# Performance work log

Hardware: AMD Instinct MI355X
Metric: run time of the kernel (lower is better)

## Reference

```python
import jax, jax.numpy as jnp
import numpy as np

NP, NR, NK = 64, 8, 500          # problems, rollouts, candidate nodes
H, HEADS, VD = 256, 8, 8         # hidden_dim, heads, vars_dim
HD = H // HEADS                  # head_dim
CLIP = 10.0                      # tanh logit clipping
NEG_INF = -jnp.inf


def setup_inputs() -> dict:
    key = jax.random.key(0)
    ks = jax.random.split(key, 17)
    f = lambda k, s: jax.random.normal(k, s, dtype=jnp.float32)
    B = NP * NR
    s = 1.0 / np.sqrt(H)
    return {
        "X": f(ks[0], (NP, NK, H)),
        "K": f(ks[1], (HEADS, NP, NK, HD)),
        "V": f(ks[2], (HEADS, NP, NK, HD)),
        "query": f(ks[3], (B, H)),
        "state1": f(ks[4], (B, H)),
        "state2": f(ks[5], (B, H)),
        "varfeat": f(ks[6], (NP, VD, NK)),
        "mask": jax.random.uniform(ks[7], (NP, NR, NK)) < 0.1,
        "nn_Q": f(ks[8], (HEADS, H, HD)) * (1.0 / np.sqrt(HD)),
        "nn_O": f(ks[9], (H, H)) * s,
        "nn_A": f(ks[10], (VD, H)) * s,
        "nn_B": f(ks[11], (H,)) * s,
        "nn_W": f(ks[12], (H,)) * s,
        "W_ih": f(ks[13], (4 * H, H)) * s,
        "W_hh": f(ks[14], (4 * H, H)) * s,
        "b_ih": f(ks[15], (4 * H,)) * s,
        "b_hh": f(ks[16], (4 * H,)) * s,
    }


def _decode(X, K, V, query, state1, state2, varfeat, mask,
            nn_Q, nn_O, nn_A, nn_B, nn_W, W_ih, W_hh, b_ih, b_hh):
    B = query.shape[0]
    # --- LSTMCell (PyTorch gate order: i, f, g, o) ---
    gates = query @ W_ih.T + b_ih + state1 @ W_hh.T + b_hh
    i, fg, g, o = jnp.split(gates, 4, axis=1)
    c = jax.nn.sigmoid(fg) * state2 + jax.nn.sigmoid(i) * jnp.tanh(g)
    h = jax.nn.sigmoid(o) * jnp.tanh(c)
    # --- MultiHeadAttention (glimpse) ---
    q = h.reshape(NP, NR, H)
    Q = jnp.einsum('pqh,ahd->apqd', q, nn_Q)                    # [heads,NP,NR,HD]
    S = jnp.einsum('apqd,apkd->apqk', Q, K) * (1.0 / np.sqrt(HD))
    S = jnp.where(mask[None], NEG_INF, S)
    S = jax.nn.softmax(S, axis=-1)
    x = jnp.einsum('apqk,apkd->apqd', S, V)
    x = x.transpose(1, 2, 0, 3).reshape(NP, NR, H)              # [NP,NR,H]
    qm = x @ nn_O                                               # glimpse query
    # --- additive attention with variable features ---
    vf = jnp.einsum('pvk,vh->pkh', varfeat, nn_A) + nn_B        # [NP,NK,H]
    t = jnp.tanh(X[:, None] + vf[:, None] + qm[:, :, None])     # [NP,NR,NK,H]
    logit = jnp.einsum('pqkh,h->pqk', t, nn_W)
    logit = jnp.where(mask, NEG_INF, logit).reshape(B, NK)
    # --- choose (mode=1: greedy argmax) ---
    infeasible = logit == NEG_INF
    l = jnp.where(infeasible, NEG_INF, jnp.tanh(logit) * CLIP)
    chosen = jnp.argmax(l, axis=1)
    logp = jax.nn.log_softmax(l, axis=1)
    chosen_p = jnp.take_along_axis(logp, chosen[:, None], axis=1).squeeze(1)
    return h, c, chosen_p


def reference(X, K, V, query, state1, state2, varfeat, mask,
              nn_Q, nn_O, nn_A, nn_B, nn_W, W_ih, W_hh, b_ih, b_hh):
    return _decode(X, K, V, query, state1, state2, varfeat, mask,
                   nn_Q, nn_O, nn_A, nn_B, nn_W, W_ih, W_hh, b_ih, b_hh)
```

## Files before the change

kernel.cpp:

```cpp
#include <hip/hip_runtime.h>

#define NPP   64
#define NRR   8
#define NKK   500
#define HDIM  256
#define NHEAD 8
#define VDIM  8
#define HD    32
#define BTOT  512

__device__ __forceinline__ float fast_tanh(float x) {
  const float e = __expf(2.f * x);
  return 1.f - 2.f * __builtin_amdgcn_rcpf(e + 1.f);
}
__device__ __forceinline__ float fast_sig(float x) {
  return __builtin_amdgcn_rcpf(1.f + __expf(-x));
}

__global__ __launch_bounds__(256) void k_lstm3(
    const float* __restrict__ query, const float* __restrict__ state1,
    const float* __restrict__ state2,
    const float* __restrict__ W_ih, const float* __restrict__ W_hh,
    const float* __restrict__ b_ih, const float* __restrict__ b_hh,
    const unsigned char* __restrict__ maskb, int* __restrict__ flagp,
    float* __restrict__ out_h, float* __restrict__ out_c)
{
  __shared__ float Wt[32][33];
  __shared__ float At[32][33];
  __shared__ float gt[32][33];

  const int t  = threadIdx.x;
  const int hb = blockIdx.x;
  const int bb = blockIdx.y;

  if (flagp != nullptr && hb == 0 && bb == 0) {
    __shared__ int f;
    if (t == 0) f = 0;
    __syncthreads();
    int any = 0;
    for (int j = t; j < 2048; j += 256) any |= maskb[2 * j + 1];
    if (any) atomicOr(&f, 1);
    __syncthreads();
    if (t == 0) *flagp = f;
  }

  const int trow = t >> 4;
  const int tcol = t & 15;

  float acc00 = 0.f, acc01 = 0.f, acc10 = 0.f, acc11 = 0.f;

  const int wrow = t >> 3, wk4 = t & 7;
  const int wpart = wrow >> 3, whh = wrow & 7;
  const int wgrow = wpart * HDIM + hb * 8 + whh;
  const int agrow = bb * 32 + wrow;

  for (int k0 = 0; k0 < 512; k0 += 32) {
    __syncthreads();
    {
      const float* wsrc = (k0 < 256) ? (W_ih + (size_t)wgrow * HDIM + k0)
                                     : (W_hh + (size_t)wgrow * HDIM + (k0 - 256));
      const float4 wv = *reinterpret_cast<const float4*>(wsrc + wk4 * 4);
      Wt[wk4 * 4 + 0][wrow] = wv.x; Wt[wk4 * 4 + 1][wrow] = wv.y;
      Wt[wk4 * 4 + 2][wrow] = wv.z; Wt[wk4 * 4 + 3][wrow] = wv.w;

      const float* asrc = (k0 < 256) ? (query  + (size_t)agrow * HDIM + k0)
                                     : (state1 + (size_t)agrow * HDIM + (k0 - 256));
      const float4 av = *reinterpret_cast<const float4*>(asrc + wk4 * 4);
      At[wk4 * 4 + 0][wrow] = av.x; At[wk4 * 4 + 1][wrow] = av.y;
      At[wk4 * 4 + 2][wrow] = av.z; At[wk4 * 4 + 3][wrow] = av.w;
    }
    __syncthreads();

#pragma unroll 8
    for (int kk = 0; kk < 32; ++kk) {
      const float w0 = Wt[kk][trow], w1 = Wt[kk][trow + 16];
      const float a0 = At[kk][tcol], a1 = At[kk][tcol + 16];
      acc00 += w0 * a0; acc01 += w0 * a1;
      acc10 += w1 * a0; acc11 += w1 * a1;
    }
  }

  gt[trow][tcol] = acc00;      gt[trow][tcol + 16] = acc01;
  gt[trow + 16][tcol] = acc10; gt[trow + 16][tcol + 16] = acc11;
  __syncthreads();

  {
    const int h = t & 7, b = t >> 3;
    const int gh = hb * 8 + h;
    const int gb = bb * 32 + b;
    const float bi = b_ih[0 * HDIM + gh] + b_hh[0 * HDIM + gh];
    const float bf = b_ih[1 * HDIM + gh] + b_hh[1 * HDIM + gh];
    const float bg = b_ih[2 * HDIM + gh] + b_hh[2 * HDIM + gh];
    const float bo = b_ih[3 * HDIM + gh] + b_hh[3 * HDIM + gh];
    const float iv = fast_sig (gt[ 0 + h][b] + bi);
    const float fv = fast_sig (gt[ 8 + h][b] + bf);
    const float gv = fast_tanh(gt[16 + h][b] + bg);
    const float ov = fast_sig (gt[24 + h][b] + bo);
    const size_t off = (size_t)gb * HDIM + gh;
    const float c = fv * state2[off] + iv * gv;
    out_c[off] = c;
    out_h[off] = ov * fast_tanh(c);
  }
}

__global__ __launch_bounds__(1024) void k_attn6(
    const float* __restrict__ Kt, const float* __restrict__ Vt,
    const float* __restrict__ nn_Q, const float* __restrict__ nn_O,
    const void* __restrict__ maskp, const int* __restrict__ flagp,
    const float* __restrict__ out_h, float* __restrict__ qmw, int use_slabs)
{
  const int p = blockIdx.x >> 3;
  const int a = blockIdx.x & 7;
  const int t = threadIdx.x;
  const int wave = t >> 6, lane = t & 63;

  __shared__ float hs[NRR][HDIM];
  __shared__ float buf[HDIM * 33];
  __shared__ float Qs[NRR][HD];
  __shared__ float Sb[NRR][NKK];
  __shared__ float xs[NRR][HD];

  const unsigned char* mb = (const unsigned char*)maskp;
  const int* mi = (const int*)maskp;

  float4 hv = make_float4(0.f, 0.f, 0.f, 0.f);
  if (t < 512)
    hv = reinterpret_cast<const float4*>(out_h + (size_t)p * NRR * HDIM)[t];
  const float4* nq4 = reinterpret_cast<const float4*>(nn_Q + (size_t)a * HDIM * HD);
  const float4 q0 = nq4[t];
  const float4 q1 = nq4[t + 1024];

  const int flag = *flagp;

  const int k2 = t >> 1, dh = t & 1;
  const int kc = (k2 < NKK) ? k2 : (NKK - 1);
  const float4 kreg = *reinterpret_cast<const float4*>(
      Kt + (((size_t)a * NPP + p) * NKK + kc) * HD + dh * 16);

  const int dpv = t & 31, kspv = t >> 5;
  const float* vb = Vt + ((size_t)a * NPP + p) * NKK * HD + dpv;
  float vreg[16];
#pragma unroll
  for (int j = 0; j < 15; ++j) vreg[j] = vb[(size_t)(kspv + 32 * j) * HD];
  vreg[15] = (kspv < NKK - 480) ? vb[(size_t)(kspv + 480) * HD] : 0.f;

  float maskval[NRR];
#pragma unroll
  for (int r = 0; r < NRR; ++r) maskval[r] = 0.f;
  if (dh == 0 && k2 < NKK) {
    if (flag) {
#pragma unroll
      for (int r = 0; r < NRR; ++r)
        maskval[r] = mb[(size_t)(p * NRR + r) * NKK + k2] ? -INFINITY : 0.f;
    } else {
#pragma unroll
      for (int r = 0; r < NRR; ++r)
        maskval[r] = mi[(size_t)(p * NRR + r) * NKK + k2] ? -INFINITY : 0.f;
    }
  }

  if (t < 512) reinterpret_cast<float4*>(&hs[0][0])[t] = hv;
  {
    const int h0 = t >> 3, d40 = t & 7;
    buf[h0 * 33 + d40 * 4 + 0] = q0.x; buf[h0 * 33 + d40 * 4 + 1] = q0.y;
    buf[h0 * 33 + d40 * 4 + 2] = q0.z; buf[h0 * 33 + d40 * 4 + 3] = q0.w;
    const int h1 = (t + 1024) >> 3, d41 = t & 7;
    buf[h1 * 33 + d41 * 4 + 0] = q1.x; buf[h1 * 33 + d41 * 4 + 1] = q1.y;
    buf[h1 * 33 + d41 * 4 + 2] = q1.z; buf[h1 * 33 + d41 * 4 + 3] = q1.w;
  }
  __syncthreads();

  {
    const int r = t >> 7, d = (t >> 2) & 31, c = t & 3;
    float acc = 0.f;
#pragma unroll 8
    for (int h = c * 64; h < c * 64 + 64; ++h)
      acc += hs[r][h] * buf[h * 33 + d];
    float* qp = &Sb[0][0];
    qp[((r * HD) + d) * 4 + c] = acc;
  }
  __syncthreads();
  if (t < 256) {
    const int r = t >> 5, d = t & 31;
    const float* qp = &Sb[0][0];
    Qs[r][d] = (qp[(r * HD + d) * 4 + 0] + qp[(r * HD + d) * 4 + 1]
              + qp[(r * HD + d) * 4 + 2] + qp[(r * HD + d) * 4 + 3])
             * 0.17677669529663687f;
  }
  __syncthreads();

  {
    float sc[NRR];
#pragma unroll
    for (int r = 0; r < NRR; ++r) sc[r] = 0.f;
#pragma unroll
    for (int c4 = 0; c4 < 4; ++c4) {
      const float u[4] = {c4 == 0 ? kreg.x : (c4 == 1 ? kreg.x : kreg.x)};
      (void)u;
    }
    {
      const float4 u = kreg;
#pragma unroll
      for (int r = 0; r < NRR; ++r) {
        sc[r] += Qs[r][dh * 16 + 0] * u.x + Qs[r][dh * 16 + 1] * u.y
               + Qs[r][dh * 16 + 2] * u.z + Qs[r][dh * 16 + 3] * u.w;
      }
    }
    const float4* kr4 = reinterpret_cast<const float4*>(
        Kt + (((size_t)a * NPP + p) * NKK + kc) * HD + dh * 16);
    const float4 u1 = kr4[1], u2 = kr4[2], u3 = kr4[3];
#pragma unroll
    for (int r = 0; r < NRR; ++r) {
      sc[r] += Qs[r][dh * 16 +  4] * u1.x + Qs[r][dh * 16 +  5] * u1.y
             + Qs[r][dh * 16 +  6] * u1.z + Qs[r][dh * 16 +  7] * u1.w
             + Qs[r][dh * 16 +  8] * u2.x + Qs[r][dh * 16 +  9] * u2.y
             + Qs[r][dh * 16 + 10] * u2.z + Qs[r][dh * 16 + 11] * u2.w
             + Qs[r][dh * 16 + 12] * u3.x + Qs[r][dh * 16 + 13] * u3.y
             + Qs[r][dh * 16 + 14] * u3.z + Qs[r][dh * 16 + 15] * u3.w;
    }
#pragma unroll
    for (int r = 0; r < NRR; ++r) sc[r] += __shfl_xor(sc[r], 1, 64);
    if (dh == 0 && k2 < NKK) {
#pragma unroll
      for (int r = 0; r < NRR; ++r)
        Sb[r][k2] = sc[r] + maskval[r];
    }
  }
  __syncthreads();

  if (wave < NRR) {
    const int r = wave;
    float m = -INFINITY;
    for (int k = lane; k < NKK; k += 64) m = fmaxf(m, Sb[r][k]);
#pragma unroll
    for (int off = 32; off > 0; off >>= 1) m = fmaxf(m, __shfl_xor(m, off, 64));
    float ssum = 0.f;
    for (int k = lane; k < NKK; k += 64) {
      const float e = __expf(Sb[r][k] - m);
      Sb[r][k] = e;
      ssum += e;
    }
#pragma unroll
    for (int off = 32; off > 0; off >>= 1) ssum += __shfl_xor(ssum, off, 64);
    const float inv = 1.f / ssum;
    for (int k = lane; k < NKK; k += 64) Sb[r][k] *= inv;
  }
  __syncthreads();

  {
    float acc[NRR];
#pragma unroll
    for (int r = 0; r < NRR; ++r) acc[r] = 0.f;
#pragma unroll
    for (int j = 0; j < 15; ++j) {
      const int k = kspv + 32 * j;
      const float v = vreg[j];
#pragma unroll
      for (int r = 0; r < NRR; ++r) acc[r] += Sb[r][k] * v;
    }
    if (kspv < NKK - 480) {
      const int k = kspv + 480;
      const float v = vreg[15];
#pragma unroll
      for (int r = 0; r < NRR; ++r) acc[r] += Sb[r][k] * v;
    }
#pragma unroll
    for (int r = 0; r < NRR; ++r) buf[(kspv * NRR + r) * HD + dpv] = acc[r];
  }
  __syncthreads();
  if (t < 256) {
    const int r = t >> 5, d = t & 31;
    float s = 0.f;
#pragma unroll
    for (int ks = 0; ks < 32; ++ks) s += buf[(ks * NRR + r) * HD + d];
    xs[r][d] = s;
  }
  __syncthreads();

  {
    const int j = t & 255, rr = t >> 8;
    const int r0 = rr * 2;
    float a0 = 0.f, a1 = 0.f;
#pragma unroll 8
    for (int d = 0; d < HD; ++d) {
      const float w = nn_O[((size_t)(a * HD + d)) * HDIM + j];
      a0 += xs[r0][d] * w;
      a1 += xs[r0 + 1][d] * w;
    }
    if (use_slabs) {
      float* slab = qmw + (size_t)a * BTOT * HDIM;
      slab[(size_t)(p * NRR + r0) * HDIM + j] = a0;
      slab[(size_t)(p * NRR + r0 + 1) * HDIM + j] = a1;
    } else {
      atomicAdd(&qmw[(size_t)(p * NRR + r0) * HDIM + j], a0);
      atomicAdd(&qmw[(size_t)(p * NRR + r0 + 1) * HDIM + j], a1);
    }
  }
}

__global__ __launch_bounds__(256) void k_logits4(
    const float* __restrict__ X, const float* __restrict__ varfeat,
    const float* __restrict__ nn_A, const float* __restrict__ nn_B,
    const float* __restrict__ nn_W, const float* __restrict__ qmw,
    int use_slabs, const int* __restrict__ flagp,
    const void* __restrict__ maskp, float* __restrict__ ls)
{
  const int p  = blockIdx.x >> 5;
  const int kt = blockIdx.x & 31;
  const int t = threadIdx.x;
  const int wave = t >> 6, lane = t & 63;
  const int h0 = lane * 4;

  __shared__ float As[VDIM][260];
  __shared__ float Ws[HDIM];
  __shared__ float qb[NRR][260];

  const unsigned char* mb = (const unsigned char*)maskp;
  const int* mi = (const int*)maskp;

  const int flag = *flagp;

  for (int idx = t; idx < VDIM * HDIM; idx += 256)
    As[idx >> 8][idx & 255] = nn_A[idx];
  Ws[t] = nn_W[t];
  for (int idx = t; idx < NRR * HDIM; idx += 256) {
    const int r = idx >> 8, h = idx & 255;
    float q;
    if (use_slabs) {
      q = 0.f;
#pragma unroll
      for (int a = 0; a < NHEAD; ++a)
        q += qmw[(size_t)a * BTOT * HDIM + (size_t)(p * NRR + r) * HDIM + h];
    } else {
      q = qmw[(size_t)(p * NRR + r) * HDIM + h];
    }
    qb[r][h] = q + nn_B[h];
  }
  __syncthreads();
  const bool mbyte = (flag != 0);

  const float4 w4 = *reinterpret_cast<const float4*>(&Ws[h0]);

  for (int kk = 0; kk < 4; ++kk) {
    const int k = kt * 16 + wave * 4 + kk;
    if (k >= NKK) break;

    const float4 x4 = *reinterpret_cast<const float4*>(
        X + ((size_t)p * NKK + k) * HDIM + h0);
    float base0 = x4.x, base1 = x4.y, base2 = x4.z, base3 = x4.w;
#pragma unroll
    for (int v = 0; v < VDIM; ++v) {
      const float vv = varfeat[((size_t)p * VDIM + v) * NKK + k];
      const float4 a4 = *reinterpret_cast<const float4*>(&As[v][h0]);
      base0 += vv * a4.x; base1 += vv * a4.y;
      base2 += vv * a4.z; base3 += vv * a4.w;
    }

    float acc[NRR];
#pragma unroll
    for (int r = 0; r < NRR; ++r) {
      const float4 q4 = *reinterpret_cast<const float4*>(&qb[r][h0]);
      acc[r] = fast_tanh(base0 + q4.x) * w4.x + fast_tanh(base1 + q4.y) * w4.y
             + fast_tanh(base2 + q4.z) * w4.z + fast_tanh(base3 + q4.w) * w4.w;
    }

    float v4[4];
    {
      float sw[8];
#pragma unroll
      for (int j = 0; j < 8; ++j) sw[j] = __shfl_xor(acc[j], 32, 64);
      const bool hi = (lane & 32) != 0;
#pragma unroll
      for (int j = 0; j < 4; ++j)
        v4[j] = hi ? (acc[j + 4] + sw[j + 4]) : (acc[j] + sw[j]);
    }
    float v2[2];
    {
      float sw[4];
#pragma unroll
      for (int j = 0; j < 4; ++j) sw[j] = __shfl_xor(v4[j], 16, 64);
      const bool hi = (lane & 16) != 0;
      v2[0] = hi ? (v4[2] + sw[2]) : (v4[0] + sw[0]);
      v2[1] = hi ? (v4[3] + sw[3]) : (v4[1] + sw[1]);
    }
    float w;
    {
      const float s0 = __shfl_xor(v2[0], 8, 64);
      const float s1 = __shfl_xor(v2[1], 8, 64);
      w = ((lane & 8) != 0) ? (v2[1] + s1) : (v2[0] + s0);
    }
    w += __shfl_xor(w, 4, 64);
    w += __shfl_xor(w, 2, 64);
    w += __shfl_xor(w, 1, 64);

    if ((lane & 7) == 0) {
      const int r = lane >> 3;
      const size_t mrow = (size_t)(p * NRR + r) * NKK + k;
      const bool mk = mbyte ? (mb[mrow] != 0) : (mi[mrow] != 0);
      ls[mrow] = mk ? -INFINITY : fast_tanh(w) * 10.0f;
    }
  }
}

__global__ __launch_bounds__(64) void k_choose(
    const float* __restrict__ ls, float* __restrict__ out_p)
{
  const int b = blockIdx.x;
  const int lane = threadIdx.x;
  float m = -INFINITY;
  float lv[8];
  int n = 0;
  for (int k = lane; k < NKK; k += 64, ++n) {
    lv[n] = ls[(size_t)b * NKK + k];
    m = fmaxf(m, lv[n]);
  }
#pragma unroll
  for (int off = 32; off > 0; off >>= 1) m = fmaxf(m, __shfl_xor(m, off, 64));
  float s = 0.f;
  for (int i = 0; i < n; ++i) s += __expf(lv[i] - m);
#pragma unroll
  for (int off = 32; off > 0; off >>= 1) s += __shfl_xor(s, off, 64);
  if (lane == 0) out_p[b] = -logf(s);
}

__global__ __launch_bounds__(256) void k_fused(
    const float* __restrict__ X, const float* __restrict__ Kt,
    const float* __restrict__ Vt, const float* __restrict__ varfeat,
    const void* __restrict__ maskp,
    const float* __restrict__ nn_Q, const float* __restrict__ nn_O,
    const float* __restrict__ nn_A, const float* __restrict__ nn_B,
    const float* __restrict__ nn_W,
    const float* __restrict__ out_h, float* __restrict__ out_p)
{
  const int p = blockIdx.x >> 3;
  const int r = blockIdx.x & 7;
  const int t = threadIdx.x;
  const int wave = t >> 6, lane = t & 63;

  __shared__ float hs[HDIM];
  __shared__ float Qs[NHEAD][HD];
  __shared__ float Sb[NHEAD][NKK];
  __shared__ float xs[HDIM];
  __shared__ float qs[HDIM];
  __shared__ float As2[HDIM][VDIM];
  __shared__ float Ws[HDIM];
  __shared__ float lsb[NKK];
  __shared__ int   mask_any;

  const unsigned char* mb = (const unsigned char*)maskp;
  if (t == 0) mask_any = 0;
  __syncthreads();
  {
    int any = 0;
    for (int j = t; j < 2048; j += 256) any |= mb[2 * j + 1];
    if (any) atomicOr(&mask_any, 1);
  }
  for (int idx = t; idx < VDIM * HDIM; idx += 256)
    As2[idx & 255][idx >> 8] = nn_A[idx];
  Ws[t] = nn_W[t];
  hs[t] = out_h[(size_t)(p * NRR + r) * HDIM + t];
  __syncthreads();
  const bool mbyte = (mask_any != 0);
  const int* mi = (const int*)maskp;
  const size_t mrow = (size_t)(p * NRR + r) * NKK;
  {
    const int a = t >> 5, d = t & 31;
    const float* nq = nn_Q + (size_t)a * HDIM * HD + d;
    float acc = 0.f;
    for (int h = 0; h < HDIM; ++h) acc += hs[h] * nq[(size_t)h * HD];
    Qs[a][d] = acc * 0.17677669529663687f;
  }
  __syncthreads();
  for (int k = t; k < NKK; k += 256) {
    const bool mk = mbyte ? (mb[mrow + k] != 0) : (mi[mrow + k] != 0);
#pragma unroll
    for (int a = 0; a < NHEAD; ++a) {
      const float4* kr4 = reinterpret_cast<const float4*>(
          Kt + (((size_t)a * NPP + p) * NKK + k) * HD);
      float s = 0.f;
#pragma unroll
      for (int d4 = 0; d4 < HD / 4; ++d4) {
        const float4 u = kr4[d4];
        s += Qs[a][4 * d4] * u.x + Qs[a][4 * d4 + 1] * u.y
           + Qs[a][4 * d4 + 2] * u.z + Qs[a][4 * d4 + 3] * u.w;
      }
      Sb[a][k] = mk ? -INFINITY : s;
    }
  }
  __syncthreads();
  for (int aa = 0; aa < 2; ++aa) {
    const int a = wave * 2 + aa;
    float m = -INFINITY;
    for (int k = lane; k < NKK; k += 64) m = fmaxf(m, Sb[a][k]);
#pragma unroll
    for (int off = 32; off > 0; off >>= 1) m = fmaxf(m, __shfl_xor(m, off, 64));
    float ssum = 0.f;
    for (int k = lane; k < NKK; k += 64) {
      const float e = expf(Sb[a][k] - m);
      Sb[a][k] = e; ssum += e;
    }
#pragma unroll
    for (int off = 32; off > 0; off >>= 1) ssum += __shfl_xor(ssum, off, 64);
    const float inv = 1.f / ssum;
    for (int k = lane; k < NKK; k += 64) Sb[a][k] *= inv;
  }
  __syncthreads();
  {
    const int a = t >> 5, d = t & 31;
    const float* vb = Vt + ((size_t)a * NPP + p) * NKK * HD + d;
    float acc = 0.f;
    for (int k = 0; k < NKK; ++k) acc += Sb[a][k] * vb[(size_t)k * HD];
    xs[a * HD + d] = acc;
  }
  __syncthreads();
  {
    float acc = 0.f;
    for (int i = 0; i < HDIM; ++i) acc += xs[i] * nn_O[(size_t)i * HDIM + t];
    qs[t] = acc + nn_B[t];
  }
  __syncthreads();
  for (int k = t; k < NKK; k += 256) {
    float vfv[VDIM];
#pragma unroll
    for (int v = 0; v < VDIM; ++v)
      vfv[v] = varfeat[((size_t)p * VDIM + v) * NKK + k];
    const float4* xp4 = reinterpret_cast<const float4*>(
        X + ((size_t)p * NKK + k) * HDIM);
    float acc = 0.f;
    for (int h4 = 0; h4 < HDIM / 4; ++h4) {
      const float4 ux = xp4[h4];
      const float xv[4] = {ux.x, ux.y, ux.z, ux.w};
#pragma unroll
      for (int j = 0; j < 4; ++j) {
        const int h = 4 * h4 + j;
        float base = xv[j] + qs[h];
        const float4 a0 = *reinterpret_cast<const float4*>(&As2[h][0]);
        const float4 a1 = *reinterpret_cast<const float4*>(&As2[h][4]);
        base += vfv[0] * a0.x + vfv[1] * a0.y + vfv[2] * a0.z + vfv[3] * a0.w
              + vfv[4] * a1.x + vfv[5] * a1.y + vfv[6] * a1.z + vfv[7] * a1.w;
        acc += tanhf(base) * Ws[h];
      }
    }
    lsb[k] = acc;
  }
  __syncthreads();
  for (int k = t; k < NKK; k += 256) {
    const bool mk = mbyte ? (mb[mrow + k] != 0) : (mi[mrow + k] != 0);
    lsb[k] = mk ? -INFINITY : tanhf(lsb[k]) * 10.0f;
  }
  __syncthreads();
  if (wave == 0) {
    float m = -INFINITY;
    for (int k = lane; k < NKK; k += 64) m = fmaxf(m, lsb[k]);
#pragma unroll
    for (int off = 32; off > 0; off >>= 1) m = fmaxf(m, __shfl_xor(m, off, 64));
    float s = 0.f;
    for (int k = lane; k < NKK; k += 64) s += expf(lsb[k] - m);
#pragma unroll
    for (int off = 32; off > 0; off >>= 1) s += __shfl_xor(s, off, 64);
    if (lane == 0) out_p[p * NRR + r] = -logf(s);
  }
}

extern "C" void kernel_launch(void* const* d_in, const int* in_sizes, int n_in,
                              void* d_out, int out_size, void* d_ws, size_t ws_size,
                              hipStream_t stream)
{
  const float* X       = (const float*)d_in[0];
  const float* Kt      = (const float*)d_in[1];
  const float* Vt      = (const float*)d_in[2];
  const float* query   = (const float*)d_in[3];
  const float* state1  = (const float*)d_in[4];
  const float* state2  = (const float*)d_in[5];
  const float* varfeat = (const float*)d_in[6];
  const void*  maskp   = d_in[7];
  const float* nn_Q    = (const float*)d_in[8];
  const float* nn_O    = (const float*)d_in[9];
  const float* nn_A    = (const float*)d_in[10];
  const float* nn_B    = (const float*)d_in[11];
  const float* nn_W    = (const float*)d_in[12];
  const float* W_ih    = (const float*)d_in[13];
  const float* W_hh    = (const float*)d_in[14];
  const float* b_ih    = (const float*)d_in[15];
  const float* b_hh    = (const float*)d_in[16];

  float* out   = (float*)d_out;
  float* out_h = out;
  float* out_c = out + (size_t)BTOT * HDIM;
  float* out_p = out + (size_t)2 * BTOT * HDIM;

  const size_t flag_bytes = 256;
  const size_t qm1_bytes  = (size_t)BTOT * HDIM * 4;
  const size_t qm8_bytes  = (size_t)NHEAD * BTOT * HDIM * 4;
  const size_t ls_bytes   = (size_t)BTOT * NKK * 4;

  const bool slabs  = ws_size >= flag_bytes + qm8_bytes + ls_bytes;
  const bool atomic = !slabs && ws_size >= flag_bytes + qm1_bytes + ls_bytes;
  int* flagp = (slabs || atomic) ? (int*)d_ws : nullptr;

  hipLaunchKernelGGL(k_lstm3, dim3(32, 16), dim3(256), 0, stream,
                     query, state1, state2, W_ih, W_hh, b_ih, b_hh,
                     (const unsigned char*)maskp, flagp, out_h, out_c);

  if (slabs || atomic) {
    float* qmw = (float*)((char*)d_ws + flag_bytes);
    float* lsw = (float*)((char*)d_ws + flag_bytes +
                          (slabs ? qm8_bytes : qm1_bytes));
    const int use_slabs = slabs ? 1 : 0;
    if (!slabs) hipMemsetAsync(qmw, 0, qm1_bytes, stream);
    hipLaunchKernelGGL(k_attn6, dim3(NPP * NHEAD), dim3(1024), 0, stream,
                       Kt, Vt, nn_Q, nn_O, maskp, flagp, out_h, qmw, use_slabs);
    hipLaunchKernelGGL(k_logits4, dim3(NPP * 32), dim3(256), 0, stream,
                       X, varfeat, nn_A, nn_B, nn_W, qmw, use_slabs, flagp,
                       maskp, lsw);
    hipLaunchKernelGGL(k_choose, dim3(BTOT), dim3(64), 0, stream,
                       lsw, out_p);
  } else {
    hipLaunchKernelGGL(k_fused, dim3(NPP * NRR), dim3(256), 0, stream,
                       X, Kt, Vt, varfeat, maskp,
                       nn_Q, nn_O, nn_A, nn_B, nn_W,
                       out_h, out_p);
  }
}
```

Measured before the change: 222.1 us.

## Split attention projections into standalone GEMMs and register-tile LSTM GEMM

Moves the per-head Q projection and the output projection out of the attention kernel into a reusable 32x32 register-tiled GEMM kernel. The attention kernel shrinks to 512 threads, keeps full K/V rows in registers and writes the per-head context to workspace. The LSTM GEMM now uses 64-thread blocks with 4x4 register tiles. The logits kernel reads weights straight into registers instead of staging them in shared memory. The aim is to cut redundant per-block projection work, the slab reduction and shared-memory traffic, at the cost of two extra launches and extra workspace round trips.

```diff
diff --git a/kernel.cpp b/kernel.cpp
--- a/kernel.cpp
+++ b/kernel.cpp
@@ -17,7 +17,7 @@
   return __builtin_amdgcn_rcpf(1.f + __expf(-x));
 }
 
-__global__ __launch_bounds__(256) void k_lstm3(
+__global__ __launch_bounds__(64) void k_lstm4(
     const float* __restrict__ query, const float* __restrict__ state1,
     const float* __restrict__ state2,
     const float* __restrict__ W_ih, const float* __restrict__ W_hh,
@@ -25,9 +25,9 @@
     const unsigned char* __restrict__ maskb, int* __restrict__ flagp,
     float* __restrict__ out_h, float* __restrict__ out_c)
 {
-  __shared__ float Wt[32][33];
-  __shared__ float At[32][33];
-  __shared__ float gt[32][33];
+  __shared__ float Wt[32][40];
+  __shared__ float At[32][40];
+  __shared__ float gt[32][40];
 
   const int t  = threadIdx.x;
   const int hb = blockIdx.x;
@@ -38,54 +38,67 @@
     if (t == 0) f = 0;
     __syncthreads();
     int any = 0;
-    for (int j = t; j < 2048; j += 256) any |= maskb[2 * j + 1];
+    for (int j = t; j < 2048; j += 64) any |= maskb[2 * j + 1];
     if (any) atomicOr(&f, 1);
     __syncthreads();
     if (t == 0) *flagp = f;
   }
 
-  const int trow = t >> 4;
-  const int tcol = t & 15;
-
-  float acc00 = 0.f, acc01 = 0.f, acc10 = 0.f, acc11 = 0.f;
-
-  const int wrow = t >> 3, wk4 = t & 7;
-  const int wpart = wrow >> 3, whh = wrow & 7;
-  const int wgrow = wpart * HDIM + hb * 8 + whh;
-  const int agrow = bb * 32 + wrow;
+  const int tr = t >> 3, tc = t & 7;
+  const int srow = t >> 1, sseg = (t & 1) * 16;
+  const int wgrow = (srow >> 3) * HDIM + hb * 8 + (srow & 7);
+  const int agrow = bb * 32 + srow;
+
+  float acc[4][4];
+#pragma unroll
+  for (int i = 0; i < 4; ++i)
+#pragma unroll
+    for (int j = 0; j < 4; ++j) acc[i][j] = 0.f;
 
   for (int k0 = 0; k0 < 512; k0 += 32) {
     __syncthreads();
     {
       const float* wsrc = (k0 < 256) ? (W_ih + (size_t)wgrow * HDIM + k0)
                                      : (W_hh + (size_t)wgrow * HDIM + (k0 - 256));
-      const float4 wv = *reinterpret_cast<const float4*>(wsrc + wk4 * 4);
-      Wt[wk4 * 4 + 0][wrow] = wv.x; Wt[wk4 * 4 + 1][wrow] = wv.y;
-      Wt[wk4 * 4 + 2][wrow] = wv.z; Wt[wk4 * 4 + 3][wrow] = wv.w;
-
       const float* asrc = (k0 < 256) ? (query  + (size_t)agrow * HDIM + k0)
                                      : (state1 + (size_t)agrow * HDIM + (k0 - 256));
-      const float4 av = *reinterpret_cast<const float4*>(asrc + wk4 * 4);
-      At[wk4 * 4 + 0][wrow] = av.x; At[wk4 * 4 + 1][wrow] = av.y;
-      At[wk4 * 4 + 2][wrow] = av.z; At[wk4 * 4 + 3][wrow] = av.w;
+#pragma unroll
+      for (int j = 0; j < 4; ++j) {
+        const float4 wv = *reinterpret_cast<const float4*>(wsrc + sseg + 4 * j);
+        const float4 av = *reinterpret_cast<const float4*>(asrc + sseg + 4 * j);
+        const int kk = sseg + 4 * j;
+        Wt[kk + 0][srow] = wv.x; Wt[kk + 1][srow] = wv.y;
+        Wt[kk + 2][srow] = wv.z; Wt[kk + 3][srow] = wv.w;
+        At[kk + 0][srow] = av.x; At[kk + 1][srow] = av.y;
+        At[kk + 2][srow] = av.z; At[kk + 3][srow] = av.w;
+      }
     }
     __syncthreads();
-
 #pragma unroll 8
     for (int kk = 0; kk < 32; ++kk) {
-      const float w0 = Wt[kk][trow], w1 = Wt[kk][trow + 16];
-      const float a0 = At[kk][tcol], a1 = At[kk][tcol + 16];
-      acc00 += w0 * a0; acc01 += w0 * a1;
-      acc10 += w1 * a0; acc11 += w1 * a1;
-    }
-  }
-
-  gt[trow][tcol] = acc00;      gt[trow][tcol + 16] = acc01;
-  gt[trow + 16][tcol] = acc10; gt[trow + 16][tcol + 16] = acc11;
-  __syncthreads();
-
-  {
-    const int h = t & 7, b = t >> 3;
+      const float4 wv = *reinterpret_cast<const float4*>(&Wt[kk][tr * 4]);
+      const float4 av = *reinterpret_cast<const float4*>(&At[kk][tc * 4]);
+      const float w[4] = {wv.x, wv.y, wv.z, wv.w};
+      const float a[4] = {av.x, av.y, av.z, av.w};
+#pragma unroll
+      for (int i = 0; i < 4; ++i)
+#pragma unroll
+        for (int j = 0; j < 4; ++j) acc[i][j] += w[i] * a[j];
+    }
+  }
+
+#pragma unroll
+  for (int i = 0; i < 4; ++i) {
+    float4 v;
+    v.x = acc[i][0]; v.y = acc[i][1]; v.z = acc[i][2]; v.w = acc[i][3];
+    *reinterpret_cast<float4*>(&gt[tr * 4 + i][tc * 4]) = v;
+  }
+  __syncthreads();
+
+#pragma unroll
+  for (int it = 0; it < 4; ++it) {
+    const int cell = t + 64 * it;
+    const int b = cell & 31, h = cell >> 5;
     const int gh = hb * 8 + h;
     const int gb = bb * 32 + b;
     const float bi = b_ih[0 * HDIM + gh] + b_hh[0 * HDIM + gh];
@@ -103,147 +116,139 @@
   }
 }
 
-__global__ __launch_bounds__(1024) void k_attn6(
+__global__ __launch_bounds__(64) void k_gemm256(
+    const float* __restrict__ A, const float* __restrict__ B,
+    float* __restrict__ C, int hstride, int ldb, float scale)
+{
+  __shared__ float At[32][40];
+  __shared__ float Bt[32][40];
+  const int t  = threadIdx.x;
+  const int ct = blockIdx.x;
+  const int rt = blockIdx.y;
+  const int tr = t >> 3, tc = t & 7;
+  const int srow = t >> 1, sseg = (t & 1) * 16;
+
+  const float* Asrc = A + ((size_t)(rt * 32 + srow)) * HDIM + sseg;
+  const float* Bsrc = B + (size_t)hstride * ct + (size_t)srow * ldb + sseg;
+
+  float acc[4][4];
+#pragma unroll
+  for (int i = 0; i < 4; ++i)
+#pragma unroll
+    for (int j = 0; j < 4; ++j) acc[i][j] = 0.f;
+
+  for (int k0 = 0; k0 < 256; k0 += 32) {
+    __syncthreads();
+#pragma unroll
+    for (int j = 0; j < 4; ++j) {
+      const float4 av = *reinterpret_cast<const float4*>(Asrc + k0 + 4 * j);
+      const int kk = sseg + 4 * j;
+      At[kk + 0][srow] = av.x; At[kk + 1][srow] = av.y;
+      At[kk + 2][srow] = av.z; At[kk + 3][srow] = av.w;
+      const float4 bv = *reinterpret_cast<const float4*>(
+          Bsrc + (size_t)k0 * ldb + 4 * j);
+      *reinterpret_cast<float4*>(&Bt[srow][sseg + 4 * j]) = bv;
+    }
+    __syncthreads();
+#pragma unroll 8
+    for (int kk = 0; kk < 32; ++kk) {
+      const float4 av = *reinterpret_cast<const float4*>(&At[kk][tr * 4]);
+      const float4 bv = *reinterpret_cast<const float4*>(&Bt[kk][tc * 4]);
+      const float a[4] = {av.x, av.y, av.z, av.w};
+      const float b[4] = {bv.x, bv.y, bv.z, bv.w};
+#pragma unroll
+      for (int i = 0; i < 4; ++i)
+#pragma unroll
+        for (int j = 0; j < 4; ++j) acc[i][j] += a[i] * b[j];
+    }
+  }
+
+  const int orow = rt * 32 + tr * 4;
+  const int ocol = ct * 32 + tc * 4;
+#pragma unroll
+  for (int i = 0; i < 4; ++i) {
+    float4 v;
+    v.x = acc[i][0] * scale; v.y = acc[i][1] * scale;
+    v.z = acc[i][2] * scale; v.w = acc[i][3] * scale;
+    *reinterpret_cast<float4*>(C + (size_t)(orow + i) * HDIM + ocol) = v;
+  }
+}
+
+__global__ __launch_bounds__(512, 4) void k_attn7(
     const float* __restrict__ Kt, const float* __restrict__ Vt,
-    const float* __restrict__ nn_Q, const float* __restrict__ nn_O,
-    const void* __restrict__ maskp, const int* __restrict__ flagp,
-    const float* __restrict__ out_h, float* __restrict__ qmw, int use_slabs)
+    const float* __restrict__ Qg, const void* __restrict__ maskp,
+    const int* __restrict__ flagp, float* __restrict__ xg)
 {
   const int p = blockIdx.x >> 3;
   const int a = blockIdx.x & 7;
   const int t = threadIdx.x;
   const int wave = t >> 6, lane = t & 63;
 
-  __shared__ float hs[NRR][HDIM];
-  __shared__ float buf[HDIM * 33];
-  __shared__ float Qs[NRR][HD];
-  __shared__ float Sb[NRR][NKK];
-  __shared__ float xs[NRR][HD];
-
-  const unsigned char* mb = (const unsigned char*)maskp;
-  const int* mi = (const int*)maskp;
-
-  float4 hv = make_float4(0.f, 0.f, 0.f, 0.f);
-  if (t < 512)
-    hv = reinterpret_cast<const float4*>(out_h + (size_t)p * NRR * HDIM)[t];
-  const float4* nq4 = reinterpret_cast<const float4*>(nn_Q + (size_t)a * HDIM * HD);
-  const float4 q0 = nq4[t];
-  const float4 q1 = nq4[t + 1024];
+  __shared__ float Sb[NRR][512];
+  __shared__ float pb[16][NRR][HD];
+
+  const int kc = (t < NKK) ? t : (NKK - 1);
+  const float4* kp4 = reinterpret_cast<const float4*>(
+      Kt + (((size_t)a * NPP + p) * NKK + kc) * HD);
+  float4 kreg[8];
+#pragma unroll
+  for (int j = 0; j < 8; ++j) kreg[j] = kp4[j];
+
+  const int dpv = t & 31, kb = t >> 5;
+  const float* vb = Vt + (((size_t)a * NPP + p) * NKK + (size_t)kb * 32) * HD + dpv;
+  float vreg[32];
+#pragma unroll
+  for (int j = 0; j < 32; ++j)
+    vreg[j] = (kb * 32 + j < NKK) ? vb[(size_t)j * HD] : 0.f;
 
   const int flag = *flagp;
-
-  const int k2 = t >> 1, dh = t & 1;
-  const int kc = (k2 < NKK) ? k2 : (NKK - 1);
-  const float4 kreg = *reinterpret_cast<const float4*>(
-      Kt + (((size_t)a * NPP + p) * NKK + kc) * HD + dh * 16);
-
-  const int dpv = t & 31, kspv = t >> 5;
-  const float* vb = Vt + ((size_t)a * NPP + p) * NKK * HD + dpv;
-  float vreg[16];
-#pragma unroll
-  for (int j = 0; j < 15; ++j) vreg[j] = vb[(size_t)(kspv + 32 * j) * HD];
-  vreg[15] = (kspv < NKK - 480) ? vb[(size_t)(kspv + 480) * HD] : 0.f;
-
-  float maskval[NRR];
-#pragma unroll
-  for (int r = 0; r < NRR; ++r) maskval[r] = 0.f;
-  if (dh == 0 && k2 < NKK) {
-    if (flag) {
-#pragma unroll
-      for (int r = 0; r < NRR; ++r)
-        maskval[r] = mb[(size_t)(p * NRR + r) * NKK + k2] ? -INFINITY : 0.f;
-    } else {
-#pragma unroll
-      for (int r = 0; r < NRR; ++r)
-        maskval[r] = mi[(size_t)(p * NRR + r) * NKK + k2] ? -INFINITY : 0.f;
-    }
-  }
-
-  if (t < 512) reinterpret_cast<float4*>(&hs[0][0])[t] = hv;
-  {
-    const int h0 = t >> 3, d40 = t & 7;
-    buf[h0 * 33 + d40 * 4 + 0] = q0.x; buf[h0 * 33 + d40 * 4 + 1] = q0.y;
-    buf[h0 * 33 + d40 * 4 + 2] = q0.z; buf[h0 * 33 + d40 * 4 + 3] = q0.w;
-    const int h1 = (t + 1024) >> 3, d41 = t & 7;
-    buf[h1 * 33 + d41 * 4 + 0] = q1.x; buf[h1 * 33 + d41 * 4 + 1] = q1.y;
-    buf[h1 * 33 + d41 * 4 + 2] = q1.z; buf[h1 * 33 + d41 * 4 + 3] = q1.w;
-  }
-  __syncthreads();
-
-  {
-    const int r = t >> 7, d = (t >> 2) & 31, c = t & 3;
-    float acc = 0.f;
-#pragma unroll 8
-    for (int h = c * 64; h < c * 64 + 64; ++h)
-      acc += hs[r][h] * buf[h * 33 + d];
-    float* qp = &Sb[0][0];
-    qp[((r * HD) + d) * 4 + c] = acc;
-  }
-  __syncthreads();
-  if (t < 256) {
-    const int r = t >> 5, d = t & 31;
-    const float* qp = &Sb[0][0];
-    Qs[r][d] = (qp[(r * HD + d) * 4 + 0] + qp[(r * HD + d) * 4 + 1]
-              + qp[(r * HD + d) * 4 + 2] + qp[(r * HD + d) * 4 + 3])
-             * 0.17677669529663687f;
-  }
-  __syncthreads();
-
-  {
-    float sc[NRR];
-#pragma unroll
-    for (int r = 0; r < NRR; ++r) sc[r] = 0.f;
-#pragma unroll
-    for (int c4 = 0; c4 < 4; ++c4) {
-      const float u[4] = {c4 == 0 ? kreg.x : (c4 == 1 ? kreg.x : kreg.x)};
-      (void)u;
-    }
-    {
-      const float4 u = kreg;
-#pragma unroll
-      for (int r = 0; r < NRR; ++r) {
-        sc[r] += Qs[r][dh * 16 + 0] * u.x + Qs[r][dh * 16 + 1] * u.y
-               + Qs[r][dh * 16 + 2] * u.z + Qs[r][dh * 16 + 3] * u.w;
-      }
-    }
-    const float4* kr4 = reinterpret_cast<const float4*>(
-        Kt + (((size_t)a * NPP + p) * NKK + kc) * HD + dh * 16);
-    const float4 u1 = kr4[1], u2 = kr4[2], u3 = kr4[3];
+  float maskv[NRR];
+  {
+    const unsigned char* mb = (const unsigned char*)maskp;
+    const int* mi = (const int*)maskp;
 #pragma unroll
     for (int r = 0; r < NRR; ++r) {
-      sc[r] += Qs[r][dh * 16 +  4] * u1.x + Qs[r][dh * 16 +  5] * u1.y
-             + Qs[r][dh * 16 +  6] * u1.z + Qs[r][dh * 16 +  7] * u1.w
-             + Qs[r][dh * 16 +  8] * u2.x + Qs[r][dh * 16 +  9] * u2.y
-             + Qs[r][dh * 16 + 10] * u2.z + Qs[r][dh * 16 + 11] * u2.w
-             + Qs[r][dh * 16 + 12] * u3.x + Qs[r][dh * 16 + 13] * u3.y
-             + Qs[r][dh * 16 + 14] * u3.z + Qs[r][dh * 16 + 15] * u3.w;
-    }
-#pragma unroll
-    for (int r = 0; r < NRR; ++r) sc[r] += __shfl_xor(sc[r], 1, 64);
-    if (dh == 0 && k2 < NKK) {
-#pragma unroll
-      for (int r = 0; r < NRR; ++r)
-        Sb[r][k2] = sc[r] + maskval[r];
-    }
-  }
-  __syncthreads();
-
-  if (wave < NRR) {
+      const size_t mo = (size_t)(p * NRR + r) * NKK + kc;
+      const bool mk = flag ? (mb[mo] != 0) : (mi[mo] != 0);
+      maskv[r] = mk ? -INFINITY : 0.f;
+    }
+  }
+
+#pragma unroll
+  for (int r = 0; r < NRR; ++r) {
+    const float4* q4 = reinterpret_cast<const float4*>(
+        Qg + ((size_t)(p * NRR + r)) * HDIM + a * HD);
+    float s = 0.f;
+#pragma unroll
+    for (int j = 0; j < 8; ++j) {
+      const float4 q = q4[j], k4 = kreg[j];
+      s += q.x * k4.x + q.y * k4.y + q.z * k4.z + q.w * k4.w;
+    }
+    Sb[r][t] = (t < NKK) ? (s + maskv[r]) : -INFINITY;
+  }
+  __syncthreads();
+
+  {
     const int r = wave;
-    float m = -INFINITY;
-    for (int k = lane; k < NKK; k += 64) m = fmaxf(m, Sb[r][k]);
+    float lv[8], m = -INFINITY;
+#pragma unroll
+    for (int i = 0; i < 8; ++i) {
+      lv[i] = Sb[r][lane + 64 * i];
+      m = fmaxf(m, lv[i]);
+    }
 #pragma unroll
     for (int off = 32; off > 0; off >>= 1) m = fmaxf(m, __shfl_xor(m, off, 64));
     float ssum = 0.f;
-    for (int k = lane; k < NKK; k += 64) {
-      const float e = __expf(Sb[r][k] - m);
-      Sb[r][k] = e;
-      ssum += e;
+#pragma unroll
+    for (int i = 0; i < 8; ++i) {
+      lv[i] = __expf(lv[i] - m);
+      ssum += lv[i];
     }
 #pragma unroll
     for (int off = 32; off > 0; off >>= 1) ssum += __shfl_xor(ssum, off, 64);
     const float inv = 1.f / ssum;
-    for (int k = lane; k < NKK; k += 64) Sb[r][k] *= inv;
+#pragma unroll
+    for (int i = 0; i < 8; ++i) Sb[r][lane + 64 * i] = lv[i] * inv;
   }
   __syncthreads();
 
@@ -252,58 +257,36 @@
 #pragma unroll
     for (int r = 0; r < NRR; ++r) acc[r] = 0.f;
 #pragma unroll
-    for (int j = 0; j < 15; ++j) {
-      const int k = kspv + 32 * j;
-      const float v = vreg[j];
-#pragma unroll
-      for (int r = 0; r < NRR; ++r) acc[r] += Sb[r][k] * v;
-    }
-    if (kspv < NKK - 480) {
-      const int k = kspv + 480;
-      const float v = vreg[15];
-#pragma unroll
-      for (int r = 0; r < NRR; ++r) acc[r] += Sb[r][k] * v;
-    }
-#pragma unroll
-    for (int r = 0; r < NRR; ++r) buf[(kspv * NRR + r) * HD + dpv] = acc[r];
-  }
-  __syncthreads();
+    for (int j4 = 0; j4 < 8; ++j4) {
+      const float v0 = vreg[j4 * 4 + 0], v1 = vreg[j4 * 4 + 1];
+      const float v2 = vreg[j4 * 4 + 2], v3 = vreg[j4 * 4 + 3];
+#pragma unroll
+      for (int r = 0; r < NRR; ++r) {
+        const float4 s4 = *reinterpret_cast<const float4*>(
+            &Sb[r][kb * 32 + j4 * 4]);
+        acc[r] += s4.x * v0 + s4.y * v1 + s4.z * v2 + s4.w * v3;
+      }
+    }
+#pragma unroll
+    for (int r = 0; r < NRR; ++r) pb[kb][r][dpv] = acc[r];
+  }
+  __syncthreads();
+
   if (t < 256) {
     const int r = t >> 5, d = t & 31;
     float s = 0.f;
 #pragma unroll
-    for (int ks = 0; ks < 32; ++ks) s += buf[(ks * NRR + r) * HD + d];
-    xs[r][d] = s;
-  }
-  __syncthreads();
-
-  {
-    const int j = t & 255, rr = t >> 8;
-    const int r0 = rr * 2;
-    float a0 = 0.f, a1 = 0.f;
-#pragma unroll 8
-    for (int d = 0; d < HD; ++d) {
-      const float w = nn_O[((size_t)(a * HD + d)) * HDIM + j];
-      a0 += xs[r0][d] * w;
-      a1 += xs[r0 + 1][d] * w;
-    }
-    if (use_slabs) {
-      float* slab = qmw + (size_t)a * BTOT * HDIM;
-      slab[(size_t)(p * NRR + r0) * HDIM + j] = a0;
-      slab[(size_t)(p * NRR + r0 + 1) * HDIM + j] = a1;
-    } else {
-      atomicAdd(&qmw[(size_t)(p * NRR + r0) * HDIM + j], a0);
-      atomicAdd(&qmw[(size_t)(p * NRR + r0 + 1) * HDIM + j], a1);
-    }
-  }
-}
-
-__global__ __launch_bounds__(256) void k_logits4(
+    for (int q = 0; q < 16; ++q) s += pb[q][r][d];
+    xg[((size_t)(p * NRR + r)) * HDIM + a * HD + d] = s;
+  }
+}
+
+__global__ __launch_bounds__(256) void k_logits5(
     const float* __restrict__ X, const float* __restrict__ varfeat,
     const float* __restrict__ nn_A, const float* __restrict__ nn_B,
-    const float* __restrict__ nn_W, const float* __restrict__ qmw,
-    int use_slabs, const int* __restrict__ flagp,
-    const void* __restrict__ maskp, float* __restrict__ ls)
+    const float* __restrict__ nn_W, const float* __restrict__ qm,
+    const int* __restrict__ flagp, const void* __restrict__ maskp,
+    float* __restrict__ ls)
 {
   const int p  = blockIdx.x >> 5;
   const int kt = blockIdx.x & 31;
@@ -311,35 +294,25 @@
   const int wave = t >> 6, lane = t & 63;
   const int h0 = lane * 4;
 
-  __shared__ float As[VDIM][260];
-  __shared__ float Ws[HDIM];
-  __shared__ float qb[NRR][260];
-
   const unsigned char* mb = (const unsigned char*)maskp;
   const int* mi = (const int*)maskp;
-
   const int flag = *flagp;
-
-  for (int idx = t; idx < VDIM * HDIM; idx += 256)
-    As[idx >> 8][idx & 255] = nn_A[idx];
-  Ws[t] = nn_W[t];
-  for (int idx = t; idx < NRR * HDIM; idx += 256) {
-    const int r = idx >> 8, h = idx & 255;
-    float q;
-    if (use_slabs) {
-      q = 0.f;
-#pragma unroll
-      for (int a = 0; a < NHEAD; ++a)
-        q += qmw[(size_t)a * BTOT * HDIM + (size_t)(p * NRR + r) * HDIM + h];
-    } else {
-      q = qmw[(size_t)(p * NRR + r) * HDIM + h];
-    }
-    qb[r][h] = q + nn_B[h];
-  }
-  __syncthreads();
   const bool mbyte = (flag != 0);
 
-  const float4 w4 = *reinterpret_cast<const float4*>(&Ws[h0]);
+  const float4 w4 = *reinterpret_cast<const float4*>(nn_W + h0);
+  const float4 b4 = *reinterpret_cast<const float4*>(nn_B + h0);
+  float4 a4r[VDIM];
+#pragma unroll
+  for (int v = 0; v < VDIM; ++v)
+    a4r[v] = *reinterpret_cast<const float4*>(nn_A + (size_t)v * HDIM + h0);
+  float4 q4r[NRR];
+#pragma unroll
+  for (int r = 0; r < NRR; ++r) {
+    const float4 q = *reinterpret_cast<const float4*>(
+        qm + (size_t)(p * NRR + r) * HDIM + h0);
+    q4r[r].x = q.x + b4.x; q4r[r].y = q.y + b4.y;
+    q4r[r].z = q.z + b4.z; q4r[r].w = q.w + b4.w;
+  }
 
   for (int kk = 0; kk < 4; ++kk) {
     const int k = kt * 16 + wave * 4 + kk;
@@ -351,17 +324,17 @@
 #pragma unroll
     for (int v = 0; v < VDIM; ++v) {
       const float vv = varfeat[((size_t)p * VDIM + v) * NKK + k];
-      const float4 a4 = *reinterpret_cast<const float4*>(&As[v][h0]);
-      base0 += vv * a4.x; base1 += vv * a4.y;
-      base2 += vv * a4.z; base3 += vv * a4.w;
+      base0 += vv * a4r[v].x; base1 += vv * a4r[v].y;
+      base2 += vv * a4r[v].z; base3 += vv * a4r[v].w;
     }
 
     float acc[NRR];
 #pragma unroll
     for (int r = 0; r < NRR; ++r) {
-      const float4 q4 = *reinterpret_cast<const float4*>(&qb[r][h0]);
-      acc[r] = fast_tanh(base0 + q4.x) * w4.x + fast_tanh(base1 + q4.y) * w4.y
-             + fast_tanh(base2 + q4.z) * w4.z + fast_tanh(base3 + q4.w) * w4.w;
+      acc[r] = fast_tanh(base0 + q4r[r].x) * w4.x
+             + fast_tanh(base1 + q4r[r].y) * w4.y
+             + fast_tanh(base2 + q4r[r].z) * w4.z
+             + fast_tanh(base3 + q4r[r].w) * w4.w;
     }
 
     float v4[4];
@@ -590,32 +563,34 @@
   float* out_p = out + (size_t)2 * BTOT * HDIM;
 
   const size_t flag_bytes = 256;
-  const size_t qm1_bytes  = (size_t)BTOT * HDIM * 4;
-  const size_t qm8_bytes  = (size_t)NHEAD * BTOT * HDIM * 4;
+  const size_t mat_bytes  = (size_t)BTOT * HDIM * 4;
   const size_t ls_bytes   = (size_t)BTOT * NKK * 4;
-
-  const bool slabs  = ws_size >= flag_bytes + qm8_bytes + ls_bytes;
-  const bool atomic = !slabs && ws_size >= flag_bytes + qm1_bytes + ls_bytes;
-  int* flagp = (slabs || atomic) ? (int*)d_ws : nullptr;
-
-  hipLaunchKernelGGL(k_lstm3, dim3(32, 16), dim3(256), 0, stream,
-                     query, state1, state2, W_ih, W_hh, b_ih, b_hh,
-                     (const unsigned char*)maskp, flagp, out_h, out_c);
-
-  if (slabs || atomic) {
-    float* qmw = (float*)((char*)d_ws + flag_bytes);
-    float* lsw = (float*)((char*)d_ws + flag_bytes +
-                          (slabs ? qm8_bytes : qm1_bytes));
-    const int use_slabs = slabs ? 1 : 0;
-    if (!slabs) hipMemsetAsync(qmw, 0, qm1_bytes, stream);
-    hipLaunchKernelGGL(k_attn6, dim3(NPP * NHEAD), dim3(1024), 0, stream,
-                       Kt, Vt, nn_Q, nn_O, maskp, flagp, out_h, qmw, use_slabs);
-    hipLaunchKernelGGL(k_logits4, dim3(NPP * 32), dim3(256), 0, stream,
-                       X, varfeat, nn_A, nn_B, nn_W, qmw, use_slabs, flagp,
-                       maskp, lsw);
+  const size_t need = flag_bytes + 3 * mat_bytes + ls_bytes;
+
+  if (ws_size >= need) {
+    int*   flagp = (int*)d_ws;
+    float* Qw  = (float*)((char*)d_ws + flag_bytes);
+    float* xw  = (float*)((char*)d_ws + flag_bytes + mat_bytes);
+    float* qmw = (float*)((char*)d_ws + flag_bytes + 2 * mat_bytes);
+    float* lsw = (float*)((char*)d_ws + flag_bytes + 3 * mat_bytes);
+
+    hipLaunchKernelGGL(k_lstm4, dim3(32, 16), dim3(64), 0, stream,
+                       query, state1, state2, W_ih, W_hh, b_ih, b_hh,
+                       (const unsigned char*)maskp, flagp, out_h, out_c);
+    hipLaunchKernelGGL(k_gemm256, dim3(8, 16), dim3(64), 0, stream,
+                       out_h, nn_Q, Qw, HDIM * HD, HD, 0.17677669529663687f);
+    hipLaunchKernelGGL(k_attn7, dim3(NPP * NHEAD), dim3(512), 0, stream,
+                       Kt, Vt, Qw, maskp, flagp, xw);
+    hipLaunchKernelGGL(k_gemm256, dim3(8, 16), dim3(64), 0, stream,
+                       xw, nn_O, qmw, HD, HDIM, 1.0f);
+    hipLaunchKernelGGL(k_logits5, dim3(NPP * 32), dim3(256), 0, stream,
+                       X, varfeat, nn_A, nn_B, nn_W, qmw, flagp, maskp, lsw);
     hipLaunchKernelGGL(k_choose, dim3(BTOT), dim3(64), 0, stream,
                        lsw, out_p);
   } else {
+    hipLaunchKernelGGL(k_lstm4, dim3(32, 16), dim3(64), 0, stream,
+                       query, state1, state2, W_ih, W_hh, b_ih, b_hh,
+                       (const unsigned char*)maskp, nullptr, out_h, out_c);
     hipLaunchKernelGGL(k_fused, dim3(NPP * NRR), dim3(256), 0, stream,
                        X, Kt, Vt, varfeat, maskp,
                        nn_Q, nn_O, nn_A, nn_B, nn_W,
```

Result: slower. 235.6 us (+6.1%).
